# Kernel tuning notes

Hardware: AMD Instinct MI355X
Metric: run time of the kernel (lower is better)

The kernel has to match this reference:

```python
import jax, jax.numpy as jnp
import numpy as np

R, A14, X, N0, N1, NH = 8192, 14, 3, 256, 256, 8
A = R * A14


def _sqrt(x):
    return (jnp.abs(x) + 1e-06) ** 0.5 * (x >= 0.0).astype(x.dtype)


def _mlp(x, layers):
    # layers: list of (w, b_or_None); leaky_relu between layers, not after last
    n = len(layers)
    for i, (w, b) in enumerate(layers):
        x = x @ w
        if b is not None:
            x = x + b
        if i < n - 1:
            x = jax.nn.leaky_relu(x)
    return x


def _lin_init(key, fan_in, fan_out):
    return jax.random.normal(key, (fan_in, fan_out), dtype=jnp.float32) / np.sqrt(fan_in)


def setup_inputs() -> dict:
    key = jax.random.key(0)
    ks = jax.random.split(key, 16)
    q = jax.random.normal(ks[0], (A, N0), dtype=jnp.float32)
    p = jax.random.normal(ks[1], (A, X, N0), dtype=jnp.float32)
    atom_mask = jax.random.randint(ks[2], (R, A14), 0, 2).astype(jnp.float32)
    # sam MLP: (N0 + N0) -> N0 -> N0 -> 2*NH
    sam_w1 = _lin_init(ks[3], 2 * N0, N0); sam_b1 = jnp.zeros((N0,), jnp.float32)
    sam_w2 = _lin_init(ks[4], N0, N0);      sam_b2 = jnp.zeros((N0,), jnp.float32)
    sam_w3 = _lin_init(ks[5], N0, 2 * NH);  sam_b3 = jnp.zeros((2 * NH,), jnp.float32)
    # zdm MLP: N0*NH -> N0 -> N0 -> N1
    zdm_w1 = _lin_init(ks[6], N0 * NH, N0); zdm_b1 = jnp.zeros((N0,), jnp.float32)
    zdm_w2 = _lin_init(ks[7], N0, N0);       zdm_b2 = jnp.zeros((N0,), jnp.float32)
    zdm_w3 = _lin_init(ks[8], N0, N1);       zdm_b3 = jnp.zeros((N1,), jnp.float32)
    # zdm_vec: N0*NH -> N1, no bias
    zdm_vec_w = _lin_init(ks[9], N0 * NH, N1)
    return dict(q=q, p=p, atom_mask=atom_mask,
                sam_w1=sam_w1, sam_b1=sam_b1, sam_w2=sam_w2, sam_b2=sam_b2,
                sam_w3=sam_w3, sam_b3=sam_b3,
                zdm_w1=zdm_w1, zdm_b1=zdm_b1, zdm_w2=zdm_w2, zdm_b2=zdm_b2,
                zdm_w3=zdm_w3, zdm_b3=zdm_b3, zdm_vec_w=zdm_vec_w)


def reference(q, p, atom_mask,
              sam_w1, sam_b1, sam_w2, sam_b2, sam_w3, sam_b3,
              zdm_w1, zdm_b1, zdm_w2, zdm_b2, zdm_w3, zdm_b3, zdm_vec_w):
    r, a14 = atom_mask.shape
    # norm(p, axis=1): sqrt of sum of squares over the vector (X) axis -> [A, C]
    z = jnp.concatenate([q, _sqrt((p * p).sum(axis=1))], axis=1)  # [A, 2*N0]
    sam_out = _mlp(z, [(sam_w1, sam_b1), (sam_w2, sam_b2), (sam_w3, sam_b3)])  # [A, 2*NH]
    sa = sam_out.reshape(r, a14, 2 * NH)
    q_ = q.reshape(r, a14, N0)
    p_ = p.reshape(r, a14, X, N0)
    # masked softmax over atoms within each residue
    logit_mask = (1.0 - atom_mask + 1e-06) / (atom_mask - 1e-06)  # [r, a14]
    aw = jax.nn.softmax(sa + logit_mask[:, :, None], axis=1)       # [r, a14, 2*NH]
    aw = aw.reshape(r, a14, NH, 2)
    qh = jnp.einsum('rac,rah->rch', q_, aw[..., 0])                # [r, N0, NH]
    ph = jnp.einsum('raxc,rah->rxch', p_, aw[..., 1])              # [r, X, N0, NH]
    qh_flat = qh.reshape(r, -1)          # [r, N0*NH]
    ph_flat = ph.reshape(r, X, -1)       # [r, X, N0*NH]
    res_mask = jnp.any(atom_mask.astype(bool), axis=-1).astype(ph_flat.dtype)
    qh_flat = qh_flat * res_mask[:, None]
    ph_flat = ph_flat * res_mask[:, None, None]
    qr = _mlp(qh_flat, [(zdm_w1, zdm_b1), (zdm_w2, zdm_b2), (zdm_w3, zdm_b3)])  # [r, N1]
    pr = ph_flat @ zdm_vec_w                                                     # [r, X, N1]
    return (qr, pr)
```

## Files before the change

kernel.cpp:

```cpp
#include <hip/hip_runtime.h>
#include <hip/hip_bf16.h>

#define R_TOT   8192
#define A14     14
#define A_TOT   (R_TOT * A14)
#define QR_ELEMS (R_TOT * 256)

typedef __attribute__((ext_vector_type(8))) short bf16x8;
typedef __attribute__((ext_vector_type(4))) float f32x4;
typedef __attribute__((ext_vector_type(4))) short short4v;

#define MFMA16(a, b, c) __builtin_amdgcn_mfma_f32_16x16x32_bf16((a), (b), (c), 0, 0, 0)

static __device__ __forceinline__ float b2f(short s) {
    return __uint_as_float(((unsigned)(unsigned short)s) << 16);
}

static __device__ __forceinline__ void wtrans_tile(
    const float* __restrict__ w, __hip_bfloat16* __restrict__ wT,
    int K, int N, int kb, int nb, float* tile )
{
    const int tx = threadIdx.x & 31, ty = threadIdx.x >> 5;
    #pragma unroll
    for (int i = 0; i < 32; i += 8) {
        int k = kb + ty + i, n = nb + tx;
        tile[(ty + i) * 33 + tx] = (k < K && n < N) ? w[(size_t)k * N + n] : 0.f;
    }
    __syncthreads();
    #pragma unroll
    for (int i = 0; i < 32; i += 8) {
        int n = nb + ty + i, k = kb + tx;
        if (n < N && k < K) wT[(size_t)n * K + k] = __float2bfloat16(tile[tx * 33 + ty + i]);
    }
}

__global__ __launch_bounds__(256) void wtrans_all_kernel(
    const float* __restrict__ sw1, __hip_bfloat16* __restrict__ wT1,
    const float* __restrict__ sw2, __hip_bfloat16* __restrict__ wT2,
    const float* __restrict__ sw3, __hip_bfloat16* __restrict__ wT3,
    const float* __restrict__ zw1, __hip_bfloat16* __restrict__ zT1,
    const float* __restrict__ zw2, __hip_bfloat16* __restrict__ zT2,
    const float* __restrict__ zw3, __hip_bfloat16* __restrict__ zT3,
    const float* __restrict__ zvw, __hip_bfloat16* __restrict__ vT)
{
    __shared__ float tile[32 * 33];
    int b = blockIdx.x;
    if (b < 128)      { wtrans_tile(sw1, wT1, 512, 256, (b % 16) * 32, (b / 16) * 32, tile); return; }
    b -= 128;
    if (b < 64)       { wtrans_tile(sw2, wT2, 256, 256, (b % 8) * 32, (b / 8) * 32, tile); return; }
    b -= 64;
    if (b < 8)        { wtrans_tile(sw3, wT3, 256, 16,  b * 32, 0, tile); return; }
    b -= 8;
    if (b < 512)      { wtrans_tile(zw1, zT1, 2048, 256, (b % 64) * 32, (b / 64) * 32, tile); return; }
    b -= 512;
    if (b < 64)       { wtrans_tile(zw2, zT2, 256, 256, (b % 8) * 32, (b / 8) * 32, tile); return; }
    b -= 64;
    if (b < 64)       { wtrans_tile(zw3, zT3, 256, 256, (b % 8) * 32, (b / 8) * 32, tile); return; }
    b -= 64;
    wtrans_tile(zvw, vT, 2048, 256, (b % 64) * 32, (b / 64) * 32, tile);
}

__global__ __launch_bounds__(256, 2) void sampool_kernel(
    const float* __restrict__ q, const float* __restrict__ p,
    const float* __restrict__ atom_mask,
    const __hip_bfloat16* __restrict__ wT1, const float* __restrict__ b1,
    const __hip_bfloat16* __restrict__ wT2, const float* __restrict__ b2,
    const __hip_bfloat16* __restrict__ wT3, const float* __restrict__ b3,
    __hip_bfloat16* __restrict__ qh, __hip_bfloat16* __restrict__ ph)
{
    __shared__ __align__(16) __hip_bfloat16 zl[64][520];
    __shared__ float sa_lds[64][16];
    __shared__ float aw_lds[2][4][14][8];

    const int tid = threadIdx.x;
    const int r0  = blockIdx.x * 4;
    const int a0  = r0 * A14;
    const int wv  = tid >> 6;
    const int l   = tid & 63;
    const int lr  = l & 15;
    const int lh  = l >> 4;
    const int nbase = wv * 64;

    #define NISSUE(RA, RB, RC, b)                                              \
        { _Pragma("unroll")                                                    \
          for (int i = 0; i < 4; ++i) {                                        \
              const int g = tid + ((b) * 4 + i) * 256;                         \
              const int m = g >> 6;                                            \
              const int cc = (g & 63) * 4;                                     \
              const int ar = a0 + m;                                           \
              const size_t arow = (size_t)((ar < A_TOT) ? ar : (A_TOT - 1));   \
              const float* base = p + arow * 768 + cc;                         \
              RA[i] = *(const float4*)(base);                                  \
              RB[i] = *(const float4*)(base + 256);                            \
              RC[i] = *(const float4*)(base + 512); } }

    #define NCONSUME(RA, RB, RC, b)                                            \
        { _Pragma("unroll")                                                    \
          for (int i = 0; i < 4; ++i) {                                        \
              const int g = tid + ((b) * 4 + i) * 256;                         \
              const int m = g >> 6;                                            \
              const int cc = (g & 63) * 4;                                     \
              __hip_bfloat16 t[4];                                             \
              t[0] = __float2bfloat16(sqrtf(RA[i].x*RA[i].x + RB[i].x*RB[i].x + RC[i].x*RC[i].x + 1e-6f)); \
              t[1] = __float2bfloat16(sqrtf(RA[i].y*RA[i].y + RB[i].y*RB[i].y + RC[i].y*RC[i].y + 1e-6f)); \
              t[2] = __float2bfloat16(sqrtf(RA[i].z*RA[i].z + RB[i].z*RB[i].z + RC[i].z*RC[i].z + 1e-6f)); \
              t[3] = __float2bfloat16(sqrtf(RA[i].w*RA[i].w + RB[i].w*RB[i].w + RC[i].w*RC[i].w + 1e-6f)); \
              *(short4v*)&zl[m][256 + cc] = *(const short4v*)t; } }

    float4 xa0[4], xb0[4], xc0[4];
    float4 xa1[4], xb1[4], xc1[4];

    NISSUE(xa0, xb0, xc0, 0);

    #pragma unroll 8
    for (int it = 0; it < 16; ++it) {
        const int g  = tid + it * 256;
        const int m  = g >> 6;
        const int c4 = (g & 63) * 4;
        const int ar = a0 + m;
        const size_t arow = (size_t)((ar < A_TOT) ? ar : (A_TOT - 1));
        const float4 v = *(const float4*)&q[arow * 256 + c4];
        __hip_bfloat16 t[4];
        t[0] = __float2bfloat16(v.x); t[1] = __float2bfloat16(v.y);
        t[2] = __float2bfloat16(v.z); t[3] = __float2bfloat16(v.w);
        *(short4v*)&zl[m][c4] = *(const short4v*)t;
    }
    __syncthreads();

    f32x4 acc[4][4] = {};
    const __hip_bfloat16* pB[4];
    #pragma unroll
    for (int nt = 0; nt < 4; ++nt)
        pB[nt] = wT1 + (size_t)(nbase + nt * 16 + lr) * 512 + lh * 8;

    #define L1_HALF(KB)                                                        \
        {                                                                      \
            bf16x8 bc[4], b1v[4];                                              \
            _Pragma("unroll")                                                  \
            for (int nt = 0; nt < 4; ++nt) {                                   \
                bc[nt]  = *(const bf16x8*)(pB[nt] + (KB));                     \
                b1v[nt] = *(const bf16x8*)(pB[nt] + (KB) + 32); }              \
            bf16x8 ac[4];                                                      \
            _Pragma("unroll")                                                  \
            for (int mf = 0; mf < 4; ++mf)                                     \
                ac[mf] = *(const bf16x8*)&zl[mf * 16 + lr][(KB) + lh * 8];     \
            _Pragma("unroll")                                                  \
            for (int k0 = 0; k0 < 256; k0 += 32) {                             \
                bf16x8 b2v[4], an[4];                                          \
                if (k0 + 64 < 256) {                                           \
                    _Pragma("unroll")                                          \
                    for (int nt = 0; nt < 4; ++nt)                             \
                        b2v[nt] = *(const bf16x8*)(pB[nt] + (KB) + k0 + 64);   \
                }                                                              \
                if (k0 + 32 < 256) {                                           \
                    _Pragma("unroll")                                          \
                    for (int mf = 0; mf < 4; ++mf)                             \
                        an[mf] = *(const bf16x8*)&zl[mf * 16 + lr][(KB) + k0 + 32 + lh * 8]; \
                }                                                              \
                _Pragma("unroll")                                              \
                for (int mf = 0; mf < 4; ++mf)                                 \
                    _Pragma("unroll")                                          \
                    for (int nt = 0; nt < 4; ++nt)                             \
                        acc[mf][nt] = MFMA16(ac[mf], bc[nt], acc[mf][nt]);     \
                _Pragma("unroll")                                              \
                for (int nt = 0; nt < 4; ++nt) { bc[nt] = b1v[nt]; b1v[nt] = b2v[nt]; } \
                _Pragma("unroll")                                              \
                for (int mf = 0; mf < 4; ++mf) ac[mf] = an[mf];                \
            }                                                                  \
        }

    L1_HALF(0);

    NISSUE(xa1, xb1, xc1, 1);
    NCONSUME(xa0, xb0, xc0, 0);
    NISSUE(xa0, xb0, xc0, 2);
    NCONSUME(xa1, xb1, xc1, 1);
    NISSUE(xa1, xb1, xc1, 3);
    NCONSUME(xa0, xb0, xc0, 2);
    NCONSUME(xa1, xb1, xc1, 3);
    __syncthreads();

    L1_HALF(256);
    __syncthreads();

    #pragma unroll
    for (int nt = 0; nt < 4; ++nt) {
        const int n = nbase + nt * 16 + lr;
        const float bv = b1[n];
        #pragma unroll
        for (int mf = 0; mf < 4; ++mf)
            #pragma unroll
            for (int v = 0; v < 4; ++v) {
                float x = acc[mf][nt][v] + bv;
                x = x >= 0.f ? x : 0.01f * x;
                zl[mf * 16 + lh * 4 + v][256 + n] = __float2bfloat16(x);
            }
    }
    __syncthreads();

    {
        f32x4 acc2[4][4] = {};
        const __hip_bfloat16* pB2[4];
        #pragma unroll
        for (int nt = 0; nt < 4; ++nt)
            pB2[nt] = wT2 + (size_t)(nbase + nt * 16 + lr) * 256 + lh * 8;
        bf16x8 bc[4], b1v[4];
        #pragma unroll
        for (int nt = 0; nt < 4; ++nt) { bc[nt]  = *(const bf16x8*)(pB2[nt]);
                                         b1v[nt] = *(const bf16x8*)(pB2[nt] + 32); }
        bf16x8 ac[4];
        #pragma unroll
        for (int mf = 0; mf < 4; ++mf)
            ac[mf] = *(const bf16x8*)&zl[mf * 16 + lr][256 + lh * 8];

        #pragma unroll
        for (int k0 = 0; k0 < 256; k0 += 32) {
            bf16x8 b2v[4], an[4];
            if (k0 + 64 < 256) {
                #pragma unroll
                for (int nt = 0; nt < 4; ++nt)
                    b2v[nt] = *(const bf16x8*)(pB2[nt] + k0 + 64);
            }
            if (k0 + 32 < 256) {
                #pragma unroll
                for (int mf = 0; mf < 4; ++mf)
                    an[mf] = *(const bf16x8*)&zl[mf * 16 + lr][256 + k0 + 32 + lh * 8];
            }
            #pragma unroll
            for (int mf = 0; mf < 4; ++mf)
                #pragma unroll
                for (int nt = 0; nt < 4; ++nt)
                    acc2[mf][nt] = MFMA16(ac[mf], bc[nt], acc2[mf][nt]);
            #pragma unroll
            for (int nt = 0; nt < 4; ++nt) { bc[nt] = b1v[nt]; b1v[nt] = b2v[nt]; }
            #pragma unroll
            for (int mf = 0; mf < 4; ++mf) ac[mf] = an[mf];
        }
        __syncthreads();
        #pragma unroll
        for (int nt = 0; nt < 4; ++nt) {
            const int n = nbase + nt * 16 + lr;
            const float bv = b2[n];
            #pragma unroll
            for (int mf = 0; mf < 4; ++mf)
                #pragma unroll
                for (int v = 0; v < 4; ++v) {
                    float x = acc2[mf][nt][v] + bv;
                    x = x >= 0.f ? x : 0.01f * x;
                    zl[mf * 16 + lh * 4 + v][256 + n] = __float2bfloat16(x);
                }
        }
    }
    __syncthreads();

    {
        f32x4 a3 = {};
        const __hip_bfloat16* pW3 = wT3 + (size_t)lr * 256 + lh * 8;
        bf16x8 bwc = *(const bf16x8*)(pW3);
        bf16x8 bw1 = *(const bf16x8*)(pW3 + 32);
        #pragma unroll
        for (int k0 = 0; k0 < 256; k0 += 32) {
            bf16x8 bw2;
            if (k0 + 64 < 256) bw2 = *(const bf16x8*)(pW3 + k0 + 64);
            const bf16x8 af = *(const bf16x8*)&zl[wv * 16 + lr][256 + k0 + lh * 8];
            a3 = MFMA16(af, bwc, a3);
            bwc = bw1; bw1 = bw2;
        }
        const float bv = b3[lr];
        #pragma unroll
        for (int v = 0; v < 4; ++v)
            sa_lds[wv * 16 + lh * 4 + v][lr] = a3[v] + bv;
    }
    __syncthreads();

    if (tid < 64) {
        const int res = tid >> 4, ch = tid & 15;
        const size_t rg = (size_t)(r0 + res);
        float sl[14];
        float mx = -3.0e38f, anym = 0.f;
        #pragma unroll
        for (int a = 0; a < 14; ++a) {
            const float m = atom_mask[rg * 14 + a];
            anym = fmaxf(anym, m);
            const float lm = (1.0f - m + 1e-6f) / (m - 1e-6f);
            const float v = sa_lds[res * 14 + a][ch] + lm;
            sl[a] = v;
            mx = fmaxf(mx, v);
        }
        float s = 0.f;
        #pragma unroll
        for (int a = 0; a < 14; ++a) { sl[a] = expf(sl[a] - mx); s += sl[a]; }
        const float inv = ((anym != 0.f) ? 1.f : 0.f) / s;
        const int h = ch >> 1;
        #pragma unroll
        for (int a = 0; a < 14; ++a)
            aw_lds[ch & 1][res][a][h] = sl[a] * inv;
    }
    __syncthreads();

    #pragma unroll
    for (int jr = 0; jr < 4; ++jr) {
        const int job = tid + jr * 256;
        const int res = job >> 8;
        const int s   = (job >> 6) & 3;
        const int c4  = (job & 63) * 4;
        const size_t rg = (size_t)(r0 + res);
        const float* const aw = &aw_lds[(s == 0) ? 0 : 1][res][0][0];
        float acc4[4][8] = {};
        if (s == 0) {
            #pragma unroll
            for (int a = 0; a < 14; ++a) {
                const short4v qv = *(const short4v*)&zl[res * 14 + a][c4];
                const float qf[4] = { b2f(qv.x), b2f(qv.y), b2f(qv.z), b2f(qv.w) };
                #pragma unroll
                for (int ci = 0; ci < 4; ++ci)
                    #pragma unroll
                    for (int h = 0; h < 8; ++h)
                        acc4[ci][h] = fmaf(qf[ci], aw[a * 8 + h], acc4[ci][h]);
            }
        } else {
            const int x = s - 1;
            #pragma unroll
            for (int a = 0; a < 14; ++a) {
                const float4 pv = *(const float4*)&p[(rg * 14 + a) * 768 + (size_t)x * 256 + c4];
                const float pf[4] = { pv.x, pv.y, pv.z, pv.w };
                #pragma unroll
                for (int ci = 0; ci < 4; ++ci)
                    #pragma unroll
                    for (int h = 0; h < 8; ++h)
                        acc4[ci][h] = fmaf(pf[ci], aw[a * 8 + h], acc4[ci][h]);
            }
        }
        alignas(16) __hip_bfloat16 tmp[32];
        #pragma unroll
        for (int ci = 0; ci < 4; ++ci)
            #pragma unroll
            for (int h = 0; h < 8; ++h)
                tmp[ci * 8 + h] = __float2bfloat16(acc4[ci][h]);
        __hip_bfloat16* const dst = (s == 0)
            ? &qh[rg * 2048 + (size_t)c4 * 8]
            : &ph[(rg * 3 + (s - 1)) * 2048 + (size_t)c4 * 8];
        #pragma unroll
        for (int u = 0; u < 4; ++u)
            *reinterpret_cast<int4*>(dst + u * 8) = *reinterpret_cast<const int4*>(tmp + u * 8);
    }
    #undef NISSUE
    #undef NCONSUME
    #undef L1_HALF
}

__global__ __launch_bounds__(256, 3) void tail_kernel(
    const __hip_bfloat16* __restrict__ qh, const __hip_bfloat16* __restrict__ ph,
    const __hip_bfloat16* __restrict__ zT1, const float* __restrict__ zb1,
    const __hip_bfloat16* __restrict__ zT2, const float* __restrict__ zb2,
    const __hip_bfloat16* __restrict__ zT3, const float* __restrict__ zb3,
    const __hip_bfloat16* __restrict__ vT,
    float* __restrict__ qr, float* __restrict__ pr)
{
    __shared__ __align__(16) __hip_bfloat16 xl[2][32][264];
    __shared__ __align__(16) __hip_bfloat16 hl[32][264];

    const int tid = threadIdx.x;
    const int wv  = tid >> 6;
    const int l   = tid & 63;
    const int lr  = l & 15;
    const int lh  = l >> 4;
    const int nbase = wv * 64;
    const bool is_zdm = (blockIdx.x < 256);
    const int a0 = (is_zdm ? blockIdx.x : (blockIdx.x - 256)) * 32;
    const __hip_bfloat16* const x = is_zdm ? qh : ph;
    const __hip_bfloat16* const w1 = is_zdm ? zT1 : vT;

    int4 st[4];
    #define LOADC(c)                                                          \
        { _Pragma("unroll")                                                   \
          for (int it = 0; it < 4; ++it) {                                    \
              const int g = tid + it * 256;                                   \
              const int m = g >> 5, c8 = (g & 31) * 8;                        \
              st[it] = *(const int4*)&x[(size_t)(a0 + m) * 2048 + (c) * 256 + c8]; } }
    #define WRITEC(buf)                                                       \
        { _Pragma("unroll")                                                   \
          for (int it = 0; it < 4; ++it) {                                    \
              const int g = tid + it * 256;                                   \
              const int m = g >> 5, c8 = (g & 31) * 8;                        \
              *(int4*)&xl[buf][m][c8] = st[it]; } }

    f32x4 acc[2][4] = {};
    {
        const __hip_bfloat16* pB[4];
        #pragma unroll
        for (int nt = 0; nt < 4; ++nt)
            pB[nt] = w1 + (size_t)(nbase + nt * 16 + lr) * 2048 + lh * 8;

        LOADC(0); WRITEC(0); __syncthreads();
        for (int c = 0; c < 8; ++c) {
            if (c < 7) LOADC(c + 1);
            const __hip_bfloat16 (* const cur)[264] = xl[c & 1];
            bf16x8 bc[4];
            #pragma unroll
            for (int nt = 0; nt < 4; ++nt) bc[nt] = *(const bf16x8*)(pB[nt] + c * 256);
            #pragma unroll
            for (int k0 = 0; k0 < 256; k0 += 32) {
                bf16x8 bn[4];
                if (k0 + 32 < 256) {
                    #pragma unroll
                    for (int nt = 0; nt < 4; ++nt)
                        bn[nt] = *(const bf16x8*)(pB[nt] + c * 256 + k0 + 32);
                }
                const int kc = k0 + lh * 8;
                const bf16x8 a0f = *(const bf16x8*)&cur[lr][kc];
                const bf16x8 a1f = *(const bf16x8*)&cur[16 + lr][kc];
                #pragma unroll
                for (int nt = 0; nt < 4; ++nt) {
                    acc[0][nt] = MFMA16(a0f, bc[nt], acc[0][nt]);
                    acc[1][nt] = MFMA16(a1f, bc[nt], acc[1][nt]);
                }
                #pragma unroll
                for (int nt = 0; nt < 4; ++nt) bc[nt] = bn[nt];
            }
            if (c < 7) WRITEC((c + 1) & 1);
            __syncthreads();
        }
    }

    if (!is_zdm) {
        #pragma unroll
        for (int nt = 0; nt < 4; ++nt) {
            const int n = nbase + nt * 16 + lr;
            #pragma unroll
            for (int mt = 0; mt < 2; ++mt)
                #pragma unroll
                for (int v = 0; v < 4; ++v)
                    pr[(size_t)(a0 + mt * 16 + lh * 4 + v) * 256 + n] = acc[mt][nt][v];
        }
        return;
    }

    #pragma unroll
    for (int nt = 0; nt < 4; ++nt) {
        const int n = nbase + nt * 16 + lr;
        const float bv = zb1[n];
        #pragma unroll
        for (int mt = 0; mt < 2; ++mt)
            #pragma unroll
            for (int v = 0; v < 4; ++v) {
                float xv = acc[mt][nt][v] + bv;
                xv = xv >= 0.f ? xv : 0.01f * xv;
                hl[mt * 16 + lh * 4 + v][n] = __float2bfloat16(xv);
            }
    }
    __syncthreads();

    {
        f32x4 acc2[2][4] = {};
        const __hip_bfloat16* pB[4];
        #pragma unroll
        for (int nt = 0; nt < 4; ++nt)
            pB[nt] = zT2 + (size_t)(nbase + nt * 16 + lr) * 256 + lh * 8;
        bf16x8 bc[4];
        #pragma unroll
        for (int nt = 0; nt < 4; ++nt) bc[nt] = *(const bf16x8*)(pB[nt]);
        #pragma unroll
        for (int k0 = 0; k0 < 256; k0 += 32) {
            bf16x8 bn[4];
            if (k0 + 32 < 256) {
                #pragma unroll
                for (int nt = 0; nt < 4; ++nt)
                    bn[nt] = *(const bf16x8*)(pB[nt] + k0 + 32);
            }
            const int kc = k0 + lh * 8;
            const bf16x8 a0f = *(const bf16x8*)&hl[lr][kc];
            const bf16x8 a1f = *(const bf16x8*)&hl[16 + lr][kc];
            #pragma unroll
            for (int nt = 0; nt < 4; ++nt) {
                acc2[0][nt] = MFMA16(a0f, bc[nt], acc2[0][nt]);
                acc2[1][nt] = MFMA16(a1f, bc[nt], acc2[1][nt]);
            }
            #pragma unroll
            for (int nt = 0; nt < 4; ++nt) bc[nt] = bn[nt];
        }
        __syncthreads();
        #pragma unroll
        for (int nt = 0; nt < 4; ++nt) {
            const int n = nbase + nt * 16 + lr;
            const float bv = zb2[n];
            #pragma unroll
            for (int mt = 0; mt < 2; ++mt)
                #pragma unroll
                for (int v = 0; v < 4; ++v) {
                    float xv = acc2[mt][nt][v] + bv;
                    xv = xv >= 0.f ? xv : 0.01f * xv;
                    hl[mt * 16 + lh * 4 + v][n] = __float2bfloat16(xv);
                }
        }
    }
    __syncthreads();

    {
        f32x4 acc3[2][4] = {};
        const __hip_bfloat16* pB[4];
        #pragma unroll
        for (int nt = 0; nt < 4; ++nt)
            pB[nt] = zT3 + (size_t)(nbase + nt * 16 + lr) * 256 + lh * 8;
        bf16x8 bc[4];
        #pragma unroll
        for (int nt = 0; nt < 4; ++nt) bc[nt] = *(const bf16x8*)(pB[nt]);
        #pragma unroll
        for (int k0 = 0; k0 < 256; k0 += 32) {
            bf16x8 bn[4];
            if (k0 + 32 < 256) {
                #pragma unroll
                for (int nt = 0; nt < 4; ++nt)
                    bn[nt] = *(const bf16x8*)(pB[nt] + k0 + 32);
            }
            const int kc = k0 + lh * 8;
            const bf16x8 a0f = *(const bf16x8*)&hl[lr][kc];
            const bf16x8 a1f = *(const bf16x8*)&hl[16 + lr][kc];
            #pragma unroll
            for (int nt = 0; nt < 4; ++nt) {
                acc3[0][nt] = MFMA16(a0f, bc[nt], acc3[0][nt]);
                acc3[1][nt] = MFMA16(a1f, bc[nt], acc3[1][nt]);
            }
            #pragma unroll
            for (int nt = 0; nt < 4; ++nt) bc[nt] = bn[nt];
        }
        #pragma unroll
        for (int nt = 0; nt < 4; ++nt) {
            const int n = nbase + nt * 16 + lr;
            const float bv = zb3[n];
            #pragma unroll
            for (int mt = 0; mt < 2; ++mt)
                #pragma unroll
                for (int v = 0; v < 4; ++v)
                    qr[(size_t)(a0 + mt * 16 + lh * 4 + v) * 256 + n] = acc3[mt][nt][v] + bv;
        }
    }
    #undef LOADC
    #undef WRITEC
}

extern "C" void kernel_launch(void* const* d_in, const int* in_sizes, int n_in,
                              void* d_out, int out_size, void* d_ws, size_t ws_size,
                              hipStream_t stream)
{
    const float* q    = (const float*)d_in[0];
    const float* p    = (const float*)d_in[1];
    const float* amsk = (const float*)d_in[2];
    const float* sw1  = (const float*)d_in[3];
    const float* sb1  = (const float*)d_in[4];
    const float* sw2  = (const float*)d_in[5];
    const float* sb2  = (const float*)d_in[6];
    const float* sw3  = (const float*)d_in[7];
    const float* sb3  = (const float*)d_in[8];
    const float* zw1  = (const float*)d_in[9];
    const float* zb1  = (const float*)d_in[10];
    const float* zw2  = (const float*)d_in[11];
    const float* zb2  = (const float*)d_in[12];
    const float* zw3  = (const float*)d_in[13];
    const float* zb3  = (const float*)d_in[14];
    const float* zvw  = (const float*)d_in[15];

    char* ws = (char*)d_ws;
    size_t off = 0;
    __hip_bfloat16* qh   = (__hip_bfloat16*)(ws + off);  off += (size_t)R_TOT * 2048 * 2;
    __hip_bfloat16* ph   = (__hip_bfloat16*)(ws + off);  off += (size_t)R_TOT * 3 * 2048 * 2;
    __hip_bfloat16* wT1  = (__hip_bfloat16*)(ws + off);  off += 256 * 512 * 2;
    __hip_bfloat16* wT2  = (__hip_bfloat16*)(ws + off);  off += 256 * 256 * 2;
    __hip_bfloat16* wT3  = (__hip_bfloat16*)(ws + off);  off += 16 * 256 * 2;
    __hip_bfloat16* zT1  = (__hip_bfloat16*)(ws + off);  off += 256 * 2048 * 2;
    __hip_bfloat16* zT2  = (__hip_bfloat16*)(ws + off);  off += 256 * 256 * 2;
    __hip_bfloat16* zT3  = (__hip_bfloat16*)(ws + off);  off += 256 * 256 * 2;
    __hip_bfloat16* vT   = (__hip_bfloat16*)(ws + off);  off += 256 * 2048 * 2;

    float* qr = (float*)d_out;
    float* pr = (float*)d_out + QR_ELEMS;

    wtrans_all_kernel<<<1352, 256, 0, stream>>>(sw1, wT1, sw2, wT2, sw3, wT3,
                                                zw1, zT1, zw2, zT2, zw3, zT3, zvw, vT);
    sampool_kernel<<<R_TOT / 4, 256, 0, stream>>>(q, p, amsk, wT1, sb1, wT2, sb2, wT3, sb3, qh, ph);
    tail_kernel<<<1024, 256, 0, stream>>>(qh, ph, zT1, zb1, zT2, zb2, zT3, zb3, vT, qr, pr);

    (void)in_sizes; (void)n_in; (void)out_size; (void)ws_size;
}
```

Baseline: 425.1 us.

## Halve sampool LDS footprint to fit four blocks per CU

Shrinks the shared staging buffer from 520 to 264 columns by reusing one 256-column region: the q half of layer 1 runs first, then a barrier, then the norm half overwrites the same space. Later layers write their activations into that same region. To make this possible, the q pooling step now re-reads fp32 q from global memory instead of the bf16 copy in LDS, and the softmax weights are stored as bf16. Launch bounds are raised to 4 blocks per CU to raise occupancy, at the cost of an extra barrier, extra global reads of q, lower-precision pooling weights, and a tighter register budget that may cause spills.

```diff
diff --git a/kernel.cpp b/kernel.cpp
--- a/kernel.cpp
+++ b/kernel.cpp
@@ -60,7 +60,7 @@
     wtrans_tile(zvw, vT, 2048, 256, (b % 64) * 32, (b / 64) * 32, tile);
 }
 
-__global__ __launch_bounds__(256, 2) void sampool_kernel(
+__global__ __launch_bounds__(256, 4) void sampool_kernel(
     const float* __restrict__ q, const float* __restrict__ p,
     const float* __restrict__ atom_mask,
     const __hip_bfloat16* __restrict__ wT1, const float* __restrict__ b1,
@@ -68,9 +68,9 @@
     const __hip_bfloat16* __restrict__ wT3, const float* __restrict__ b3,
     __hip_bfloat16* __restrict__ qh, __hip_bfloat16* __restrict__ ph)
 {
-    __shared__ __align__(16) __hip_bfloat16 zl[64][520];
+    __shared__ __align__(16) __hip_bfloat16 zl[64][264];
     __shared__ float sa_lds[64][16];
-    __shared__ float aw_lds[2][4][14][8];
+    __shared__ __align__(16) __hip_bfloat16 aw_lds[2][4][14][8];
 
     const int tid = threadIdx.x;
     const int r0  = blockIdx.x * 4;
@@ -105,7 +105,7 @@
               t[1] = __float2bfloat16(sqrtf(RA[i].y*RA[i].y + RB[i].y*RB[i].y + RC[i].y*RC[i].y + 1e-6f)); \
               t[2] = __float2bfloat16(sqrtf(RA[i].z*RA[i].z + RB[i].z*RB[i].z + RC[i].z*RC[i].z + 1e-6f)); \
               t[3] = __float2bfloat16(sqrtf(RA[i].w*RA[i].w + RB[i].w*RB[i].w + RC[i].w*RC[i].w + 1e-6f)); \
-              *(short4v*)&zl[m][256 + cc] = *(const short4v*)t; } }
+              *(short4v*)&zl[m][cc] = *(const short4v*)t; } }
 
     float4 xa0[4], xb0[4], xc0[4];
     float4 xa1[4], xb1[4], xc1[4];
@@ -143,7 +143,7 @@
             bf16x8 ac[4];                                                      \
             _Pragma("unroll")                                                  \
             for (int mf = 0; mf < 4; ++mf)                                     \
-                ac[mf] = *(const bf16x8*)&zl[mf * 16 + lr][(KB) + lh * 8];     \
+                ac[mf] = *(const bf16x8*)&zl[mf * 16 + lr][lh * 8];            \
             _Pragma("unroll")                                                  \
             for (int k0 = 0; k0 < 256; k0 += 32) {                             \
                 bf16x8 b2v[4], an[4];                                          \
@@ -155,7 +155,7 @@
                 if (k0 + 32 < 256) {                                           \
                     _Pragma("unroll")                                          \
                     for (int mf = 0; mf < 4; ++mf)                             \
-                        an[mf] = *(const bf16x8*)&zl[mf * 16 + lr][(KB) + k0 + 32 + lh * 8]; \
+                        an[mf] = *(const bf16x8*)&zl[mf * 16 + lr][k0 + 32 + lh * 8]; \
                 }                                                              \
                 _Pragma("unroll")                                              \
                 for (int mf = 0; mf < 4; ++mf)                                 \
@@ -170,6 +170,7 @@
         }
 
     L1_HALF(0);
+    __syncthreads();
 
     NISSUE(xa1, xb1, xc1, 1);
     NCONSUME(xa0, xb0, xc0, 0);
@@ -193,7 +194,7 @@
             for (int v = 0; v < 4; ++v) {
                 float x = acc[mf][nt][v] + bv;
                 x = x >= 0.f ? x : 0.01f * x;
-                zl[mf * 16 + lh * 4 + v][256 + n] = __float2bfloat16(x);
+                zl[mf * 16 + lh * 4 + v][n] = __float2bfloat16(x);
             }
     }
     __syncthreads();
@@ -211,7 +212,7 @@
         bf16x8 ac[4];
         #pragma unroll
         for (int mf = 0; mf < 4; ++mf)
-            ac[mf] = *(const bf16x8*)&zl[mf * 16 + lr][256 + lh * 8];
+            ac[mf] = *(const bf16x8*)&zl[mf * 16 + lr][lh * 8];
 
         #pragma unroll
         for (int k0 = 0; k0 < 256; k0 += 32) {
@@ -224,7 +225,7 @@
             if (k0 + 32 < 256) {
                 #pragma unroll
                 for (int mf = 0; mf < 4; ++mf)
-                    an[mf] = *(const bf16x8*)&zl[mf * 16 + lr][256 + k0 + 32 + lh * 8];
+                    an[mf] = *(const bf16x8*)&zl[mf * 16 + lr][k0 + 32 + lh * 8];
             }
             #pragma unroll
             for (int mf = 0; mf < 4; ++mf)
@@ -247,7 +248,7 @@
                 for (int v = 0; v < 4; ++v) {
                     float x = acc2[mf][nt][v] + bv;
                     x = x >= 0.f ? x : 0.01f * x;
-                    zl[mf * 16 + lh * 4 + v][256 + n] = __float2bfloat16(x);
+                    zl[mf * 16 + lh * 4 + v][n] = __float2bfloat16(x);
                 }
         }
     }
@@ -262,7 +263,7 @@
         for (int k0 = 0; k0 < 256; k0 += 32) {
             bf16x8 bw2;
             if (k0 + 64 < 256) bw2 = *(const bf16x8*)(pW3 + k0 + 64);
-            const bf16x8 af = *(const bf16x8*)&zl[wv * 16 + lr][256 + k0 + lh * 8];
+            const bf16x8 af = *(const bf16x8*)&zl[wv * 16 + lr][k0 + lh * 8];
             a3 = MFMA16(af, bwc, a3);
             bwc = bw1; bw1 = bw2;
         }
@@ -294,7 +295,7 @@
         const int h = ch >> 1;
         #pragma unroll
         for (int a = 0; a < 14; ++a)
-            aw_lds[ch & 1][res][a][h] = sl[a] * inv;
+            aw_lds[ch & 1][res][a][h] = __float2bfloat16(sl[a] * inv);
     }
     __syncthreads();
 
@@ -305,31 +306,25 @@
         const int s   = (job >> 6) & 3;
         const int c4  = (job & 63) * 4;
         const size_t rg = (size_t)(r0 + res);
-        const float* const aw = &aw_lds[(s == 0) ? 0 : 1][res][0][0];
+        const __hip_bfloat16* const awp = &aw_lds[(s == 0) ? 0 : 1][res][0][0];
+        const float* src;
+        size_t stride;
+        if (s == 0) { src = &q[(rg * 14) * 256 + c4]; stride = 256; }
+        else        { src = &p[(rg * 14) * 768 + (size_t)(s - 1) * 256 + c4]; stride = 768; }
         float acc4[4][8] = {};
-        if (s == 0) {
-            #pragma unroll
-            for (int a = 0; a < 14; ++a) {
-                const short4v qv = *(const short4v*)&zl[res * 14 + a][c4];
-                const float qf[4] = { b2f(qv.x), b2f(qv.y), b2f(qv.z), b2f(qv.w) };
-                #pragma unroll
-                for (int ci = 0; ci < 4; ++ci)
-                    #pragma unroll
-                    for (int h = 0; h < 8; ++h)
-                        acc4[ci][h] = fmaf(qf[ci], aw[a * 8 + h], acc4[ci][h]);
-            }
-        } else {
-            const int x = s - 1;
-            #pragma unroll
-            for (int a = 0; a < 14; ++a) {
-                const float4 pv = *(const float4*)&p[(rg * 14 + a) * 768 + (size_t)x * 256 + c4];
-                const float pf[4] = { pv.x, pv.y, pv.z, pv.w };
-                #pragma unroll
-                for (int ci = 0; ci < 4; ++ci)
-                    #pragma unroll
-                    for (int h = 0; h < 8; ++h)
-                        acc4[ci][h] = fmaf(pf[ci], aw[a * 8 + h], acc4[ci][h]);
-            }
+        #pragma unroll
+        for (int a = 0; a < 14; ++a) {
+            const float4 v = *(const float4*)(src + (size_t)a * stride);
+            const float vf[4] = { v.x, v.y, v.z, v.w };
+            const short4v w0 = *(const short4v*)&awp[a * 8];
+            const short4v w1 = *(const short4v*)&awp[a * 8 + 4];
+            const float wf[8] = { b2f(w0.x), b2f(w0.y), b2f(w0.z), b2f(w0.w),
+                                  b2f(w1.x), b2f(w1.y), b2f(w1.z), b2f(w1.w) };
+            #pragma unroll
+            for (int ci = 0; ci < 4; ++ci)
+                #pragma unroll
+                for (int h = 0; h < 8; ++h)
+                    acc4[ci][h] = fmaf(vf[ci], wf[h], acc4[ci][h]);
         }
         alignas(16) __hip_bfloat16 tmp[32];
         #pragma unroll
```

Result: slower. 1.178 ms (+177.0%).
